# Kernel optimization log

Measured on AMD Instinct MI355X. Metric: run time of the kernel, lower is better.

## Reference

```python
import jax, jax.numpy as jnp
import numpy as np

H = 128          # hidden_channels
N_USER = 500000
N_ANIME = 20000
N_EDGE = 500000


def setup_inputs() -> dict:
    key = jax.random.key(0)
    k = jax.random.split(key, 8)
    s1 = 1.0 / np.sqrt(2 * H)   # torch Linear init scale (uniform bound)
    s2 = 1.0 / np.sqrt(H)
    return {
        "z_user": jax.random.normal(k[0], (N_USER, H), dtype=jnp.float32),
        "z_anime": jax.random.normal(k[1], (N_ANIME, H), dtype=jnp.float32),
        "row": jax.random.randint(k[2], (N_EDGE,), 0, N_USER, dtype=jnp.int64 if jax.config.jax_enable_x64 else jnp.int32),
        "col": jax.random.randint(k[3], (N_EDGE,), 0, N_ANIME, dtype=jnp.int64 if jax.config.jax_enable_x64 else jnp.int32),
        "W1": jax.random.uniform(k[4], (2 * H, H), minval=-s1, maxval=s1, dtype=jnp.float32),
        "b1": jnp.zeros((H,), dtype=jnp.float32),
        "W2": jax.random.uniform(k[5], (H, 1), minval=-s2, maxval=s2, dtype=jnp.float32),
        "b2": jnp.zeros((1,), dtype=jnp.float32),
    }


def reference(z_user, z_anime, row, col, W1, b1, W2, b2):
    zu = z_user[row]            # [E, H] gather
    za = z_anime[col]           # [E, H] gather
    # cat([zu, za], -1) @ W1 == zu @ W1[:H] + za @ W1[H:]  (avoids materializing concat)
    h = zu @ W1[:H] + za @ W1[H:] + b1          # [E, H]
    h = jax.nn.relu(h)
    out = h @ W2 + b2                            # [E, 1]
    return out.reshape(-1)
```

## Files before the change

### kernel.cpp

```cpp
#include <hip/hip_runtime.h>
#include <hip/hip_bf16.h>
#include <stdint.h>

#define H_ 128
#define THREADS 256
#define EDGES_PER_BLOCK 128

typedef __bf16 bf16x8 __attribute__((ext_vector_type(8)));
typedef float  f32x4  __attribute__((ext_vector_type(4)));


__device__ inline bf16x8 pack8(float4 a, float4 b) {
    bf16x8 v;
    v[0] = (__bf16)a.x; v[1] = (__bf16)a.y; v[2] = (__bf16)a.z; v[3] = (__bf16)a.w;
    v[4] = (__bf16)b.x; v[5] = (__bf16)b.y; v[6] = (__bf16)b.z; v[7] = (__bf16)b.w;
    return v;
}

__global__ void prep_kernel(const float* __restrict__ W1,
                            const float* __restrict__ za,
                            __bf16* __restrict__ wfrag,
                            __bf16* __restrict__ za_bf,
                            int nza) {
    int t = blockIdx.x * 256 + threadIdx.x;
    if (t < 32768) {
        int j  = t & 7;
        int ln = (t >> 3) & 63;
        int nt = (t >> 9) & 7;
        int ks = (t >> 12) & 7;
        int k  = ks * 32 + ((ln >> 4) << 3) + j;
        int n  = nt * 16 + (ln & 15);
        wfrag[t] = (__bf16)W1[k * H_ + n];
    } else {
        long i = (long)(t - 32768) * 8;
        if (i < nza) {
            float4 a = *(const float4*)(za + i);
            float4 b = *(const float4*)(za + i + 4);
            *(bf16x8*)(za_bf + i) = pack8(a, b);
        }
    }
}

__global__ __launch_bounds__(THREADS, 3)
void edge_decoder_kernel(const float* __restrict__ z_user,
                         const float* __restrict__ z_anime,
                         const int*   __restrict__ row,
                         const int*   __restrict__ col,
                         const float* __restrict__ W1,
                         const float* __restrict__ b1,
                         const float* __restrict__ W2,
                         const float* __restrict__ b2,
                         const __bf16* __restrict__ wfrag,
                         const __bf16* __restrict__ za_bf,
                         int use_ws,
                         float* __restrict__ out,
                         int E) {
    __shared__ bf16x8 Bf[4][8][64];

    const int tid  = threadIdx.x;
    const int lane = tid & 63;
    const int wv   = tid >> 6;
    const int g    = lane >> 4;
    const int m    = lane & 15;
    const int base = blockIdx.x * EDGES_PER_BLOCK + wv * 32;

    int e0 = base + m;        int e0c = e0 < E ? e0 : 0;
    int e1 = base + 16 + m;   int e1c = e1 < E ? e1 : 0;
    const int r0 = row[e0c], c0 = col[e0c];
    const int r1 = row[e1c], c1 = col[e1c];

    bf16x8 Au0[4], Au1[4];
    {
        const float* zu0 = z_user + (size_t)r0 * H_ + g * 8;
        const float* zu1 = z_user + (size_t)r1 * H_ + g * 8;
        #pragma unroll
        for (int ks = 0; ks < 4; ++ks) {
            float4 x0 = *(const float4*)(zu0 + ks * 32);
            float4 y0 = *(const float4*)(zu0 + ks * 32 + 4);
            float4 x1 = *(const float4*)(zu1 + ks * 32);
            float4 y1 = *(const float4*)(zu1 + ks * 32 + 4);
            Au0[ks] = pack8(x0, y0);
            Au1[ks] = pack8(x1, y1);
        }
    }

    if (use_ws) {
        const int4* src = (const int4*)wfrag;
        int4*       dst = (int4*)&Bf[0][0][0];
        #pragma unroll
        for (int i = 0; i < 8; ++i)
            dst[tid + i * THREADS] = src[tid + i * THREADS];
    } else {
        __bf16* d = (__bf16*)&Bf[0][0][0];
        for (int idx = tid; idx < H_ * H_; idx += THREADS) {
            int k = idx >> 7, n = idx & 127;
            int ks = k >> 5, gg = (k >> 3) & 3, j = k & 7;
            int nt = n >> 4, ln = (gg << 4) | (n & 15);
            d[ks * 4096 + nt * 512 + ln * 8 + j] = (__bf16)W1[k * H_ + n];
        }
    }
    __syncthreads();

    f32x4 acc0[8], acc1[8];
    #pragma unroll
    for (int nt = 0; nt < 8; ++nt) {
        acc0[nt] = (f32x4){0.f, 0.f, 0.f, 0.f};
        acc1[nt] = (f32x4){0.f, 0.f, 0.f, 0.f};
    }

    #pragma unroll
    for (int nt = 0; nt < 8; ++nt) {
        #pragma unroll
        for (int ks = 0; ks < 4; ++ks) {
            bf16x8 b = Bf[ks][nt][lane];
            acc0[nt] = __builtin_amdgcn_mfma_f32_16x16x32_bf16(Au0[ks], b, acc0[nt], 0, 0, 0);
            acc1[nt] = __builtin_amdgcn_mfma_f32_16x16x32_bf16(Au1[ks], b, acc1[nt], 0, 0, 0);
        }
    }

    bf16x8 Aa0[4], Aa1[4];
    if (use_ws) {
        const __bf16* za0 = za_bf + (size_t)c0 * H_ + g * 8;
        const __bf16* za1 = za_bf + (size_t)c1 * H_ + g * 8;
        #pragma unroll
        for (int ks = 0; ks < 4; ++ks) {
            Aa0[ks] = *(const bf16x8*)(za0 + ks * 32);
            Aa1[ks] = *(const bf16x8*)(za1 + ks * 32);
        }
    } else {
        const float* za0 = z_anime + (size_t)c0 * H_ + g * 8;
        const float* za1 = z_anime + (size_t)c1 * H_ + g * 8;
        #pragma unroll
        for (int ks = 0; ks < 4; ++ks) {
            float4 x0 = *(const float4*)(za0 + ks * 32);
            float4 y0 = *(const float4*)(za0 + ks * 32 + 4);
            float4 x1 = *(const float4*)(za1 + ks * 32);
            float4 y1 = *(const float4*)(za1 + ks * 32 + 4);
            Aa0[ks] = pack8(x0, y0);
            Aa1[ks] = pack8(x1, y1);
        }
    }

    __syncthreads();

    if (use_ws) {
        const int4* src = (const int4*)wfrag + 2048;
        int4*       dst = (int4*)&Bf[0][0][0];
        #pragma unroll
        for (int i = 0; i < 8; ++i)
            dst[tid + i * THREADS] = src[tid + i * THREADS];
    } else {
        __bf16* d = (__bf16*)&Bf[0][0][0];
        for (int idx = tid; idx < H_ * H_; idx += THREADS) {
            int k = idx >> 7, n = idx & 127;
            int ks = k >> 5, gg = (k >> 3) & 3, j = k & 7;
            int nt = n >> 4, ln = (gg << 4) | (n & 15);
            d[ks * 4096 + nt * 512 + ln * 8 + j] = (__bf16)W1[(H_ + k) * H_ + n];
        }
    }
    __syncthreads();

    #pragma unroll
    for (int nt = 0; nt < 8; ++nt) {
        #pragma unroll
        for (int ks = 0; ks < 4; ++ks) {
            bf16x8 b = Bf[ks][nt][lane];
            acc0[nt] = __builtin_amdgcn_mfma_f32_16x16x32_bf16(Aa0[ks], b, acc0[nt], 0, 0, 0);
            acc1[nt] = __builtin_amdgcn_mfma_f32_16x16x32_bf16(Aa1[ks], b, acc1[nt], 0, 0, 0);
        }
    }

    float w2v[8], b1v[8];
    #pragma unroll
    for (int nt = 0; nt < 8; ++nt) {
        int ch = nt * 16 + m;
        w2v[nt] = W2[ch];
        b1v[nt] = b1[ch];
    }
    const float bb = b2[0];

    #pragma unroll
    for (int tile = 0; tile < 2; ++tile) {
        float ps[4];
        #pragma unroll
        for (int r = 0; r < 4; ++r) {
            float s = 0.f;
            #pragma unroll
            for (int nt = 0; nt < 8; ++nt) {
                f32x4 a = tile ? acc1[nt] : acc0[nt];
                float h = a[r] + b1v[nt];
                s = fmaf(fmaxf(h, 0.f), w2v[nt], s);
            }
            ps[r] = s;
        }
        #pragma unroll
        for (int off = 1; off < 16; off <<= 1) {
            #pragma unroll
            for (int r = 0; r < 4; ++r)
                ps[r] += __shfl_xor(ps[r], off, 64);
        }
        if (m == 0) {
            int eb = base + tile * 16 + g * 4;
            if (eb < E) {
                float4 o = make_float4(ps[0] + bb, ps[1] + bb, ps[2] + bb, ps[3] + bb);
                *(float4*)(out + eb) = o;
            }
        }
    }
}

extern "C" void kernel_launch(void* const* d_in, const int* in_sizes, int n_in,
                              void* d_out, int out_size, void* d_ws, size_t ws_size,
                              hipStream_t stream) {
    const float* z_user  = (const float*)d_in[0];
    const float* z_anime = (const float*)d_in[1];
    const int*   row     = (const int*)d_in[2];
    const int*   col     = (const int*)d_in[3];
    const float* W1      = (const float*)d_in[4];
    const float* b1      = (const float*)d_in[5];
    const float* W2      = (const float*)d_in[6];
    const float* b2      = (const float*)d_in[7];
    float*       out     = (float*)d_out;
    const int E   = in_sizes[2];
    const int nza = in_sizes[1];

    const size_t wfrag_bytes = 2u * H_ * H_ * sizeof(__bf16);
    const size_t need = wfrag_bytes + (size_t)nza * sizeof(__bf16);
    int use_ws = (d_ws != nullptr && ws_size >= need) ? 1 : 0;

    __bf16* wfrag = (__bf16*)d_ws;
    __bf16* za_bf = (__bf16*)((char*)d_ws + wfrag_bytes);

    if (use_ws) {
        int za_threads = (nza + 7) / 8;
        int nb_prep = 128 + (za_threads + 255) / 256;
        prep_kernel<<<nb_prep, 256, 0, stream>>>(W1, z_anime, wfrag, za_bf, nza);
    }

    int nb = (E + EDGES_PER_BLOCK - 1) / EDGES_PER_BLOCK;
    edge_decoder_kernel<<<nb, THREADS, 0, stream>>>(
        z_user, z_anime, row, col, W1, b1, W2, b2, wfrag, za_bf, use_ws, out, E);
}
```

Before: 82.30 us.

## Bucket-sort edges by user row before decoding to improve gather locality

Adds a histogram, scan and scatter pass that reorders edges by coarse user-row bucket, then has the decoder read the permuted row/col indices and scatter outputs back through a permutation array. The aim is for each block's z_user gathers to land in nearby memory, improving cache and DRAM locality. In exchange it adds three extra launches, a memset, global atomics and scattered output writes. With uniformly random rows over a 256MB table, the locality gain may be small against the extra passes.

Measured after the change: 170.1 us. 2.07x slower.

```diff
diff --git a/kernel.cpp b/kernel.cpp
--- a/kernel.cpp
+++ b/kernel.cpp
@@ -5,6 +5,7 @@
 #define H_ 128
 #define THREADS 256
 #define EDGES_PER_BLOCK 128
+#define NBUCKET 4096
 
 typedef __bf16 bf16x8 __attribute__((ext_vector_type(8)));
 typedef float  f32x4  __attribute__((ext_vector_type(4)));
@@ -41,11 +42,67 @@
     }
 }
 
+__global__ void hist_kernel(const int* __restrict__ row, int* __restrict__ hist,
+                            int E, int shift) {
+    int i = blockIdx.x * blockDim.x + threadIdx.x;
+    int stride = gridDim.x * blockDim.x;
+    for (; i < E; i += stride)
+        atomicAdd(&hist[row[i] >> shift], 1);
+}
+
+__global__ __launch_bounds__(1024)
+void scan_kernel(int* __restrict__ h) {
+    __shared__ int wsum[16];
+    int tid = threadIdx.x;
+    int4 v = *(int4*)(h + tid * 4);
+    int s = v.x + v.y + v.z + v.w;
+    int lane = tid & 63, wv = tid >> 6;
+    int inc = s;
+    #pragma unroll
+    for (int off = 1; off < 64; off <<= 1) {
+        int t = __shfl_up(inc, off, 64);
+        if (lane >= off) inc += t;
+    }
+    if (lane == 63) wsum[wv] = inc;
+    __syncthreads();
+    if (wv == 0) {
+        int ws = (lane < 16) ? wsum[lane] : 0;
+        #pragma unroll
+        for (int off = 1; off < 16; off <<= 1) {
+            int t = __shfl_up(ws, off, 64);
+            if (lane >= off) ws += t;
+        }
+        if (lane < 16) wsum[lane] = ws;
+    }
+    __syncthreads();
+    int waveoff = (wv > 0) ? wsum[wv - 1] : 0;
+    int excl = waveoff + inc - s;
+    int4 o;
+    o.x = excl; o.y = excl + v.x; o.z = o.y + v.y; o.w = o.z + v.z;
+    *(int4*)(h + tid * 4) = o;
+}
+
+__global__ void scatter_kernel(const int* __restrict__ row, const int* __restrict__ col,
+                               int* __restrict__ hist,
+                               int* __restrict__ rowp, int* __restrict__ colp,
+                               int* __restrict__ perm, int E, int shift) {
+    int i = blockIdx.x * blockDim.x + threadIdx.x;
+    int stride = gridDim.x * blockDim.x;
+    for (; i < E; i += stride) {
+        int r = row[i], c = col[i];
+        int pos = atomicAdd(&hist[r >> shift], 1);
+        rowp[pos] = r;
+        colp[pos] = c;
+        perm[pos] = i;
+    }
+}
+
 __global__ __launch_bounds__(THREADS, 3)
 void edge_decoder_kernel(const float* __restrict__ z_user,
                          const float* __restrict__ z_anime,
-                         const int*   __restrict__ row,
-                         const int*   __restrict__ col,
+                         const int*   __restrict__ rowp,
+                         const int*   __restrict__ colp,
+                         const int*   __restrict__ perm,
                          const float* __restrict__ W1,
                          const float* __restrict__ b1,
                          const float* __restrict__ W2,
@@ -66,8 +123,8 @@
 
     int e0 = base + m;        int e0c = e0 < E ? e0 : 0;
     int e1 = base + 16 + m;   int e1c = e1 < E ? e1 : 0;
-    const int r0 = row[e0c], c0 = col[e0c];
-    const int r1 = row[e1c], c1 = col[e1c];
+    const int r0 = rowp[e0c], c0 = colp[e0c];
+    const int r1 = rowp[e1c], c1 = colp[e1c];
 
     bf16x8 Au0[4], Au1[4];
     {
@@ -201,7 +258,19 @@
         }
         if (m == 0) {
             int eb = base + tile * 16 + g * 4;
-            if (eb < E) {
+            if (perm) {
+                if (eb + 3 < E) {
+                    int4 p = *(const int4*)(perm + eb);
+                    out[p.x] = ps[0] + bb;
+                    out[p.y] = ps[1] + bb;
+                    out[p.z] = ps[2] + bb;
+                    out[p.w] = ps[3] + bb;
+                } else {
+                    #pragma unroll
+                    for (int r = 0; r < 4; ++r)
+                        if (eb + r < E) out[perm[eb + r]] = ps[r] + bb;
+                }
+            } else if (eb < E) {
                 float4 o = make_float4(ps[0] + bb, ps[1] + bb, ps[2] + bb, ps[3] + bb);
                 *(float4*)(out + eb) = o;
             }
@@ -223,21 +292,47 @@
     float*       out     = (float*)d_out;
     const int E   = in_sizes[2];
     const int nza = in_sizes[1];
+    const int nu  = in_sizes[0] / H_;
+
+    const int nb   = (E + EDGES_PER_BLOCK - 1) / EDGES_PER_BLOCK;
+    const int Epad = nb * EDGES_PER_BLOCK;
 
     const size_t wfrag_bytes = 2u * H_ * H_ * sizeof(__bf16);
-    const size_t need = wfrag_bytes + (size_t)nza * sizeof(__bf16);
+    const size_t za_bytes    = (size_t)nza * sizeof(__bf16);
+    const size_t hist_bytes  = (size_t)NBUCKET * sizeof(int);
+    const size_t idx_bytes   = (size_t)Epad * sizeof(int);
+    const size_t need = wfrag_bytes + za_bytes + hist_bytes + 3 * idx_bytes;
     int use_ws = (d_ws != nullptr && ws_size >= need) ? 1 : 0;
 
-    __bf16* wfrag = (__bf16*)d_ws;
-    __bf16* za_bf = (__bf16*)((char*)d_ws + wfrag_bytes);
+    char* p = (char*)d_ws;
+    __bf16* wfrag = (__bf16*)p;                 p += wfrag_bytes;
+    __bf16* za_bf = (__bf16*)p;                 p += za_bytes;
+    int*    hist  = (int*)p;                    p += hist_bytes;
+    int*    rowp  = (int*)p;                    p += idx_bytes;
+    int*    colp  = (int*)p;                    p += idx_bytes;
+    int*    perm  = (int*)p;
 
     if (use_ws) {
+        int shift = 0;
+        while ((nu >> shift) >= NBUCKET) shift++;
+
+        hipMemsetAsync(hist, 0, hist_bytes, stream);
+
         int za_threads = (nza + 7) / 8;
         int nb_prep = 128 + (za_threads + 255) / 256;
         prep_kernel<<<nb_prep, 256, 0, stream>>>(W1, z_anime, wfrag, za_bf, nza);
-    }
-
-    int nb = (E + EDGES_PER_BLOCK - 1) / EDGES_PER_BLOCK;
-    edge_decoder_kernel<<<nb, THREADS, 0, stream>>>(
-        z_user, z_anime, row, col, W1, b1, W2, b2, wfrag, za_bf, use_ws, out, E);
-}
+
+        int gsb = min(1024, (E + 255) / 256);
+        hist_kernel<<<gsb, 256, 0, stream>>>(row, hist, E, shift);
+        scan_kernel<<<1, 1024, 0, stream>>>(hist);
+        scatter_kernel<<<gsb, 256, 0, stream>>>(row, col, hist, rowp, colp, perm, E, shift);
+
+        edge_decoder_kernel<<<nb, THREADS, 0, stream>>>(
+            z_user, z_anime, rowp, colp, perm, W1, b1, W2, b2,
+            wfrag, za_bf, 1, out, E);
+    } else {
+        edge_decoder_kernel<<<nb, THREADS, 0, stream>>>(
+            z_user, z_anime, row, col, nullptr, W1, b1, W2, b2,
+            wfrag, za_bf, 0, out, E);
+    }
+}
```

## Persistent kernel with double-buffered async LDS gather of user embeddings

Applied to the files above, without the earlier changes.

Replaces the one-shot-per-block launch with a persistent grid of 256 blocks, 3 waves each. Every wave loops over 32-edge tiles and loads both W1 halves into LDS once. User rows are gathered asynchronously with global_load_lds into a swizzled, double-buffered LDS area, and row/col indices are prefetched two tiles ahead, so gather latency overlaps the MFMA work. The cost is fewer resident waves (launch bounds of 1, about 160KB of LDS), a full vmcnt(0) wait at the start of each iteration, and a fixed grid size that may not fill the device.

New measurement: 106.0 us. 1.29x slower.

```diff
diff --git a/kernel.cpp b/kernel.cpp
--- a/kernel.cpp
+++ b/kernel.cpp
@@ -3,8 +3,10 @@
 #include <stdint.h>
 
 #define H_ 128
-#define THREADS 256
-#define EDGES_PER_BLOCK 128
+#define NW 3
+#define THREADS (NW * 64)
+#define TILE_E 32
+#define NBLOCKS 256
 
 typedef __bf16 bf16x8 __attribute__((ext_vector_type(8)));
 typedef float  f32x4  __attribute__((ext_vector_type(4)));
@@ -41,7 +43,11 @@
     }
 }
 
-__global__ __launch_bounds__(THREADS, 3)
+#define GLD16(gp, lp) __builtin_amdgcn_global_load_lds(                      \
+    (const __attribute__((address_space(1))) void*)(gp),                     \
+    (__attribute__((address_space(3))) void*)(lp), 16, 0, 0)
+
+__global__ __launch_bounds__(THREADS, 1)
 void edge_decoder_kernel(const float* __restrict__ z_user,
                          const float* __restrict__ z_anime,
                          const int*   __restrict__ row,
@@ -55,44 +61,22 @@
                          int use_ws,
                          float* __restrict__ out,
                          int E) {
-    __shared__ bf16x8 Bf[4][8][64];
+    __shared__ bf16x8 Bf[8][8][64];
+    __shared__ float  ZU[NW][2][TILE_E * H_];
 
     const int tid  = threadIdx.x;
     const int lane = tid & 63;
     const int wv   = tid >> 6;
     const int g    = lane >> 4;
     const int m    = lane & 15;
-    const int base = blockIdx.x * EDGES_PER_BLOCK + wv * 32;
-
-    int e0 = base + m;        int e0c = e0 < E ? e0 : 0;
-    int e1 = base + 16 + m;   int e1c = e1 < E ? e1 : 0;
-    const int r0 = row[e0c], c0 = col[e0c];
-    const int r1 = row[e1c], c1 = col[e1c];
-
-    bf16x8 Au0[4], Au1[4];
-    {
-        const float* zu0 = z_user + (size_t)r0 * H_ + g * 8;
-        const float* zu1 = z_user + (size_t)r1 * H_ + g * 8;
-        #pragma unroll
-        for (int ks = 0; ks < 4; ++ks) {
-            float4 x0 = *(const float4*)(zu0 + ks * 32);
-            float4 y0 = *(const float4*)(zu0 + ks * 32 + 4);
-            float4 x1 = *(const float4*)(zu1 + ks * 32);
-            float4 y1 = *(const float4*)(zu1 + ks * 32 + 4);
-            Au0[ks] = pack8(x0, y0);
-            Au1[ks] = pack8(x1, y1);
-        }
-    }
 
     if (use_ws) {
         const int4* src = (const int4*)wfrag;
         int4*       dst = (int4*)&Bf[0][0][0];
-        #pragma unroll
-        for (int i = 0; i < 8; ++i)
-            dst[tid + i * THREADS] = src[tid + i * THREADS];
+        for (int i = tid; i < 4096; i += THREADS) dst[i] = src[i];
     } else {
         __bf16* d = (__bf16*)&Bf[0][0][0];
-        for (int idx = tid; idx < H_ * H_; idx += THREADS) {
+        for (int idx = tid; idx < 2 * H_ * H_; idx += THREADS) {
             int k = idx >> 7, n = idx & 127;
             int ks = k >> 5, gg = (k >> 3) & 3, j = k & 7;
             int nt = n >> 4, ln = (gg << 4) | (n & 15);
@@ -101,111 +85,175 @@
     }
     __syncthreads();
 
-    f32x4 acc0[8], acc1[8];
-    #pragma unroll
-    for (int nt = 0; nt < 8; ++nt) {
-        acc0[nt] = (f32x4){0.f, 0.f, 0.f, 0.f};
-        acc1[nt] = (f32x4){0.f, 0.f, 0.f, 0.f};
-    }
-
-    #pragma unroll
-    for (int nt = 0; nt < 8; ++nt) {
-        #pragma unroll
-        for (int ks = 0; ks < 4; ++ks) {
-            bf16x8 b = Bf[ks][nt][lane];
-            acc0[nt] = __builtin_amdgcn_mfma_f32_16x16x32_bf16(Au0[ks], b, acc0[nt], 0, 0, 0);
-            acc1[nt] = __builtin_amdgcn_mfma_f32_16x16x32_bf16(Au1[ks], b, acc1[nt], 0, 0, 0);
-        }
-    }
-
-    bf16x8 Aa0[4], Aa1[4];
-    if (use_ws) {
-        const __bf16* za0 = za_bf + (size_t)c0 * H_ + g * 8;
-        const __bf16* za1 = za_bf + (size_t)c1 * H_ + g * 8;
-        #pragma unroll
-        for (int ks = 0; ks < 4; ++ks) {
-            Aa0[ks] = *(const bf16x8*)(za0 + ks * 32);
-            Aa1[ks] = *(const bf16x8*)(za1 + ks * 32);
-        }
-    } else {
-        const float* za0 = z_anime + (size_t)c0 * H_ + g * 8;
-        const float* za1 = z_anime + (size_t)c1 * H_ + g * 8;
-        #pragma unroll
-        for (int ks = 0; ks < 4; ++ks) {
-            float4 x0 = *(const float4*)(za0 + ks * 32);
-            float4 y0 = *(const float4*)(za0 + ks * 32 + 4);
-            float4 x1 = *(const float4*)(za1 + ks * 32);
-            float4 y1 = *(const float4*)(za1 + ks * 32 + 4);
-            Aa0[ks] = pack8(x0, y0);
-            Aa1[ks] = pack8(x1, y1);
-        }
-    }
-
-    __syncthreads();
-
-    if (use_ws) {
-        const int4* src = (const int4*)wfrag + 2048;
-        int4*       dst = (int4*)&Bf[0][0][0];
-        #pragma unroll
-        for (int i = 0; i < 8; ++i)
-            dst[tid + i * THREADS] = src[tid + i * THREADS];
-    } else {
-        __bf16* d = (__bf16*)&Bf[0][0][0];
-        for (int idx = tid; idx < H_ * H_; idx += THREADS) {
-            int k = idx >> 7, n = idx & 127;
-            int ks = k >> 5, gg = (k >> 3) & 3, j = k & 7;
-            int nt = n >> 4, ln = (gg << 4) | (n & 15);
-            d[ks * 4096 + nt * 512 + ln * 8 + j] = (__bf16)W1[(H_ + k) * H_ + n];
-        }
-    }
-    __syncthreads();
-
-    #pragma unroll
-    for (int nt = 0; nt < 8; ++nt) {
-        #pragma unroll
-        for (int ks = 0; ks < 4; ++ks) {
-            bf16x8 b = Bf[ks][nt][lane];
-            acc0[nt] = __builtin_amdgcn_mfma_f32_16x16x32_bf16(Aa0[ks], b, acc0[nt], 0, 0, 0);
-            acc1[nt] = __builtin_amdgcn_mfma_f32_16x16x32_bf16(Aa1[ks], b, acc1[nt], 0, 0, 0);
-        }
-    }
-
     float w2v[8], b1v[8];
     #pragma unroll
-    for (int nt = 0; nt < 8; ++nt) {
-        int ch = nt * 16 + m;
-        w2v[nt] = W2[ch];
-        b1v[nt] = b1[ch];
-    }
+    for (int nt = 0; nt < 8; ++nt) { int ch = nt * 16 + m; w2v[nt] = W2[ch]; b1v[nt] = b1[ch]; }
     const float bb = b2[0];
 
-    #pragma unroll
-    for (int tile = 0; tile < 2; ++tile) {
-        float ps[4];
-        #pragma unroll
-        for (int r = 0; r < 4; ++r) {
-            float s = 0.f;
-            #pragma unroll
-            for (int nt = 0; nt < 8; ++nt) {
-                f32x4 a = tile ? acc1[nt] : acc0[nt];
-                float h = a[r] + b1v[nt];
-                s = fmaf(fmaxf(h, 0.f), w2v[nt], s);
-            }
-            ps[r] = s;
-        }
-        #pragma unroll
-        for (int off = 1; off < 16; off <<= 1) {
-            #pragma unroll
-            for (int r = 0; r < 4; ++r)
-                ps[r] += __shfl_xor(ps[r], off, 64);
-        }
-        if (m == 0) {
-            int eb = base + tile * 16 + g * 4;
-            if (eb < E) {
-                float4 o = make_float4(ps[0] + bb, ps[1] + bb, ps[2] + bb, ps[3] + bb);
-                *(float4*)(out + eb) = o;
-            }
-        }
+    const int T = (E + TILE_E - 1) / TILE_E;
+    const int NSTREAM = gridDim.x * NW;
+    int t = blockIdx.x * NW + wv;
+    if (t >= T) return;
+
+    float* zbuf0 = &ZU[wv][0][0];
+    float* zbuf1 = &ZU[wv][1][0];
+
+    int tb = t * TILE_E;
+    int ei = tb + (lane & 31); if (ei >= E) ei = E - 1;
+    int rv = row[ei];
+    int e0 = tb + m;      if (e0 >= E) e0 = E - 1;
+    int e1 = tb + 16 + m; if (e1 >= E) e1 = E - 1;
+    int ca0 = col[e0], ca1 = col[e1];
+
+    {
+        #pragma unroll
+        for (int i = 0; i < 16; ++i) {
+            int r0 = __builtin_amdgcn_readlane(rv, 2 * i);
+            int r1 = __builtin_amdgcn_readlane(rv, 2 * i + 1);
+            int r  = (lane < 32) ? r0 : r1;
+            int e  = 2 * i + (lane >> 5);
+            int c  = (lane & 31) ^ (e & 7);
+            GLD16(z_user + (size_t)r * H_ + c * 4, zbuf0 + i * 256);
+        }
+    }
+
+    int t1 = t + NSTREAM;
+    int tbn = (t1 < T ? t1 : 0) * TILE_E;
+    int en = tbn + (lane & 31); if (en >= E) en = E - 1;
+    int rv1 = row[en];
+    int f0 = tbn + m;      if (f0 >= E) f0 = E - 1;
+    int f1 = tbn + 16 + m; if (f1 >= E) f1 = E - 1;
+    int cb0 = col[f0], cb1 = col[f1];
+
+    int cur = 0;
+    while (true) {
+        asm volatile("s_waitcnt vmcnt(0)" ::: "memory");
+
+        const int nxt = t + NSTREAM;
+        const bool have_next = (nxt < T);
+        float* zb  = cur ? zbuf1 : zbuf0;
+        float* zbn = cur ? zbuf0 : zbuf1;
+
+        bf16x8 Aa0[4], Aa1[4];
+        if (use_ws) {
+            const __bf16* p0 = za_bf + (size_t)ca0 * H_ + g * 8;
+            const __bf16* p1 = za_bf + (size_t)ca1 * H_ + g * 8;
+            #pragma unroll
+            for (int ks = 0; ks < 4; ++ks) {
+                Aa0[ks] = *(const bf16x8*)(p0 + ks * 32);
+                Aa1[ks] = *(const bf16x8*)(p1 + ks * 32);
+            }
+        } else {
+            const float* p0 = z_anime + (size_t)ca0 * H_ + g * 8;
+            const float* p1 = z_anime + (size_t)ca1 * H_ + g * 8;
+            #pragma unroll
+            for (int ks = 0; ks < 4; ++ks) {
+                Aa0[ks] = pack8(*(const float4*)(p0 + ks * 32), *(const float4*)(p0 + ks * 32 + 4));
+                Aa1[ks] = pack8(*(const float4*)(p1 + ks * 32), *(const float4*)(p1 + ks * 32 + 4));
+            }
+        }
+
+        bf16x8 Au0[4], Au1[4];
+        {
+            const int swz = m & 7;
+            const float* r0p = zb + m * H_;
+            const float* r1p = zb + (m + 16) * H_;
+            #pragma unroll
+            for (int ks = 0; ks < 4; ++ks) {
+                int c0 = g * 2 + ks * 8;
+                float4 x0 = *(const float4*)(r0p + (((c0    ) ^ swz) << 2));
+                float4 y0 = *(const float4*)(r0p + (((c0 + 1) ^ swz) << 2));
+                float4 x1 = *(const float4*)(r1p + (((c0    ) ^ swz) << 2));
+                float4 y1 = *(const float4*)(r1p + (((c0 + 1) ^ swz) << 2));
+                Au0[ks] = pack8(x0, y0);
+                Au1[ks] = pack8(x1, y1);
+            }
+        }
+
+        if (have_next) {
+            #pragma unroll
+            for (int i = 0; i < 16; ++i) {
+                int r0 = __builtin_amdgcn_readlane(rv1, 2 * i);
+                int r1 = __builtin_amdgcn_readlane(rv1, 2 * i + 1);
+                int r  = (lane < 32) ? r0 : r1;
+                int e  = 2 * i + (lane >> 5);
+                int c  = (lane & 31) ^ (e & 7);
+                GLD16(z_user + (size_t)r * H_ + c * 4, zbn + i * 256);
+            }
+        }
+
+        int t2 = t + 2 * NSTREAM;
+        int tb2 = (t2 < T ? t2 : 0) * TILE_E;
+        int e2 = tb2 + (lane & 31); if (e2 >= E) e2 = E - 1;
+        int rv2 = row[e2];
+        int h0 = tb2 + m;      if (h0 >= E) h0 = E - 1;
+        int h1 = tb2 + 16 + m; if (h1 >= E) h1 = E - 1;
+        int cc0 = col[h0], cc1 = col[h1];
+
+        f32x4 acc0[8], acc1[8];
+        #pragma unroll
+        for (int nt = 0; nt < 8; ++nt) {
+            acc0[nt] = (f32x4){0.f, 0.f, 0.f, 0.f};
+            acc1[nt] = (f32x4){0.f, 0.f, 0.f, 0.f};
+        }
+        #pragma unroll
+        for (int nt = 0; nt < 8; ++nt) {
+            #pragma unroll
+            for (int ks = 0; ks < 4; ++ks) {
+                bf16x8 b = Bf[ks][nt][lane];
+                acc0[nt] = __builtin_amdgcn_mfma_f32_16x16x32_bf16(Au0[ks], b, acc0[nt], 0, 0, 0);
+                acc1[nt] = __builtin_amdgcn_mfma_f32_16x16x32_bf16(Au1[ks], b, acc1[nt], 0, 0, 0);
+            }
+        }
+        #pragma unroll
+        for (int nt = 0; nt < 8; ++nt) {
+            #pragma unroll
+            for (int ks = 0; ks < 4; ++ks) {
+                bf16x8 b = Bf[4 + ks][nt][lane];
+                acc0[nt] = __builtin_amdgcn_mfma_f32_16x16x32_bf16(Aa0[ks], b, acc0[nt], 0, 0, 0);
+                acc1[nt] = __builtin_amdgcn_mfma_f32_16x16x32_bf16(Aa1[ks], b, acc1[nt], 0, 0, 0);
+            }
+        }
+
+        int tb0 = t * TILE_E;
+        #pragma unroll
+        for (int tile = 0; tile < 2; ++tile) {
+            float ps[4];
+            #pragma unroll
+            for (int r = 0; r < 4; ++r) {
+                float s = 0.f;
+                #pragma unroll
+                for (int nt = 0; nt < 8; ++nt) {
+                    f32x4 a = tile ? acc1[nt] : acc0[nt];
+                    float h = a[r] + b1v[nt];
+                    s = fmaf(fmaxf(h, 0.f), w2v[nt], s);
+                }
+                ps[r] = s;
+            }
+            #pragma unroll
+            for (int off = 1; off < 16; off <<= 1) {
+                #pragma unroll
+                for (int r = 0; r < 4; ++r)
+                    ps[r] += __shfl_xor(ps[r], off, 64);
+            }
+            if (m == 0) {
+                int eb = tb0 + tile * 16 + g * 4;
+                if (eb + 3 < E) {
+                    float4 o = make_float4(ps[0] + bb, ps[1] + bb, ps[2] + bb, ps[3] + bb);
+                    *(float4*)(out + eb) = o;
+                } else {
+                    #pragma unroll
+                    for (int r = 0; r < 4; ++r)
+                        if (eb + r < E) out[eb + r] = ps[r] + bb;
+                }
+            }
+        }
+
+        if (!have_next) break;
+        t = nxt; cur ^= 1;
+        rv1 = rv2;
+        ca0 = cb0; ca1 = cb1;
+        cb0 = cc0; cb1 = cc1;
     }
 }
 
@@ -237,7 +285,7 @@
         prep_kernel<<<nb_prep, 256, 0, stream>>>(W1, z_anime, wfrag, za_bf, nza);
     }
 
-    int nb = (E + EDGES_PER_BLOCK - 1) / EDGES_PER_BLOCK;
-    edge_decoder_kernel<<<nb, THREADS, 0, stream>>>(
-        z_user, z_anime, row, col, W1, b1, W2, b2, wfrag, za_bf, use_ws, out, E);
-}
+    edge_decoder_kernel<<<NBLOCKS, THREADS, 0, stream>>>(
+        z_user, z_anime, row, col, W1, b1, W2, b2,
+        wfrag, za_bf, use_ws, out, E);
+}
```

## Halve edges per wave and issue all gathers before weight staging

Applied to the files above, without the earlier changes.

Each wave now handles one 16-edge tile instead of two, so each block covers 64 edges and the grid doubles. The z_user and bf16 z_anime gathers plus the bias and W2 loads are issued up front, before the shared-memory weight copy, to hide gather latency. The launch-bounds occupancy hint rises from 3 to 4. The cost is twice as many blocks, each restaging both 32 KB weight halves into LDS, which doubles weight traffic per edge. The tail store is fixed to write scalars when fewer than four edges remain.

Measured after the change: 78.23 us. 1.05x faster.

```diff
diff --git a/kernel.cpp b/kernel.cpp
--- a/kernel.cpp
+++ b/kernel.cpp
@@ -4,7 +4,7 @@
 
 #define H_ 128
 #define THREADS 256
-#define EDGES_PER_BLOCK 128
+#define EPB 64
 
 typedef __bf16 bf16x8 __attribute__((ext_vector_type(8)));
 typedef float  f32x4  __attribute__((ext_vector_type(4)));
@@ -41,7 +41,7 @@
     }
 }
 
-__global__ __launch_bounds__(THREADS, 3)
+__global__ __launch_bounds__(THREADS, 4)
 void edge_decoder_kernel(const float* __restrict__ z_user,
                          const float* __restrict__ z_anime,
                          const int*   __restrict__ row,
@@ -62,27 +62,32 @@
     const int wv   = tid >> 6;
     const int g    = lane >> 4;
     const int m    = lane & 15;
-    const int base = blockIdx.x * EDGES_PER_BLOCK + wv * 32;
-
-    int e0 = base + m;        int e0c = e0 < E ? e0 : 0;
-    int e1 = base + 16 + m;   int e1c = e1 < E ? e1 : 0;
-    const int r0 = row[e0c], c0 = col[e0c];
-    const int r1 = row[e1c], c1 = col[e1c];
-
-    bf16x8 Au0[4], Au1[4];
+    const int base = blockIdx.x * EPB + wv * 16;
+
+    int e = base + m; if (e >= E) e = E - 1;
+    const int r0 = row[e], c0 = col[e];
+
+    float4 xu[8];
     {
-        const float* zu0 = z_user + (size_t)r0 * H_ + g * 8;
-        const float* zu1 = z_user + (size_t)r1 * H_ + g * 8;
+        const float* zu = z_user + (size_t)r0 * H_ + g * 8;
         #pragma unroll
         for (int ks = 0; ks < 4; ++ks) {
-            float4 x0 = *(const float4*)(zu0 + ks * 32);
-            float4 y0 = *(const float4*)(zu0 + ks * 32 + 4);
-            float4 x1 = *(const float4*)(zu1 + ks * 32);
-            float4 y1 = *(const float4*)(zu1 + ks * 32 + 4);
-            Au0[ks] = pack8(x0, y0);
-            Au1[ks] = pack8(x1, y1);
-        }
-    }
+            xu[2 * ks]     = *(const float4*)(zu + ks * 32);
+            xu[2 * ks + 1] = *(const float4*)(zu + ks * 32 + 4);
+        }
+    }
+    bf16x8 Aa[4];
+    if (use_ws) {
+        const __bf16* za = za_bf + (size_t)c0 * H_ + g * 8;
+        #pragma unroll
+        for (int ks = 0; ks < 4; ++ks)
+            Aa[ks] = *(const bf16x8*)(za + ks * 32);
+    }
+
+    float w2v[8], b1v[8];
+    #pragma unroll
+    for (int nt = 0; nt < 8; ++nt) { int ch = nt * 16 + m; w2v[nt] = W2[ch]; b1v[nt] = b1[ch]; }
+    const float bb = b2[0];
 
     if (use_ws) {
         const int4* src = (const int4*)wfrag;
@@ -101,44 +106,30 @@
     }
     __syncthreads();
 
-    f32x4 acc0[8], acc1[8];
-    #pragma unroll
-    for (int nt = 0; nt < 8; ++nt) {
-        acc0[nt] = (f32x4){0.f, 0.f, 0.f, 0.f};
-        acc1[nt] = (f32x4){0.f, 0.f, 0.f, 0.f};
-    }
+    bf16x8 Au[4];
+    #pragma unroll
+    for (int ks = 0; ks < 4; ++ks)
+        Au[ks] = pack8(xu[2 * ks], xu[2 * ks + 1]);
+
+    f32x4 acc[8];
+    #pragma unroll
+    for (int nt = 0; nt < 8; ++nt) acc[nt] = (f32x4){0.f, 0.f, 0.f, 0.f};
 
     #pragma unroll
     for (int nt = 0; nt < 8; ++nt) {
         #pragma unroll
         for (int ks = 0; ks < 4; ++ks) {
             bf16x8 b = Bf[ks][nt][lane];
-            acc0[nt] = __builtin_amdgcn_mfma_f32_16x16x32_bf16(Au0[ks], b, acc0[nt], 0, 0, 0);
-            acc1[nt] = __builtin_amdgcn_mfma_f32_16x16x32_bf16(Au1[ks], b, acc1[nt], 0, 0, 0);
-        }
-    }
-
-    bf16x8 Aa0[4], Aa1[4];
-    if (use_ws) {
-        const __bf16* za0 = za_bf + (size_t)c0 * H_ + g * 8;
-        const __bf16* za1 = za_bf + (size_t)c1 * H_ + g * 8;
-        #pragma unroll
-        for (int ks = 0; ks < 4; ++ks) {
-            Aa0[ks] = *(const bf16x8*)(za0 + ks * 32);
-            Aa1[ks] = *(const bf16x8*)(za1 + ks * 32);
-        }
-    } else {
-        const float* za0 = z_anime + (size_t)c0 * H_ + g * 8;
-        const float* za1 = z_anime + (size_t)c1 * H_ + g * 8;
-        #pragma unroll
-        for (int ks = 0; ks < 4; ++ks) {
-            float4 x0 = *(const float4*)(za0 + ks * 32);
-            float4 y0 = *(const float4*)(za0 + ks * 32 + 4);
-            float4 x1 = *(const float4*)(za1 + ks * 32);
-            float4 y1 = *(const float4*)(za1 + ks * 32 + 4);
-            Aa0[ks] = pack8(x0, y0);
-            Aa1[ks] = pack8(x1, y1);
-        }
+            acc[nt] = __builtin_amdgcn_mfma_f32_16x16x32_bf16(Au[ks], b, acc[nt], 0, 0, 0);
+        }
+    }
+
+    if (!use_ws) {
+        const float* za = z_anime + (size_t)c0 * H_ + g * 8;
+        #pragma unroll
+        for (int ks = 0; ks < 4; ++ks)
+            Aa[ks] = pack8(*(const float4*)(za + ks * 32),
+                           *(const float4*)(za + ks * 32 + 4));
     }
 
     __syncthreads();
@@ -165,46 +156,36 @@
         #pragma unroll
         for (int ks = 0; ks < 4; ++ks) {
             bf16x8 b = Bf[ks][nt][lane];
-            acc0[nt] = __builtin_amdgcn_mfma_f32_16x16x32_bf16(Aa0[ks], b, acc0[nt], 0, 0, 0);
-            acc1[nt] = __builtin_amdgcn_mfma_f32_16x16x32_bf16(Aa1[ks], b, acc1[nt], 0, 0, 0);
-        }
-    }
-
-    float w2v[8], b1v[8];
-    #pragma unroll
-    for (int nt = 0; nt < 8; ++nt) {
-        int ch = nt * 16 + m;
-        w2v[nt] = W2[ch];
-        b1v[nt] = b1[ch];
-    }
-    const float bb = b2[0];
-
-    #pragma unroll
-    for (int tile = 0; tile < 2; ++tile) {
-        float ps[4];
-        #pragma unroll
-        for (int r = 0; r < 4; ++r) {
-            float s = 0.f;
-            #pragma unroll
-            for (int nt = 0; nt < 8; ++nt) {
-                f32x4 a = tile ? acc1[nt] : acc0[nt];
-                float h = a[r] + b1v[nt];
-                s = fmaf(fmaxf(h, 0.f), w2v[nt], s);
-            }
-            ps[r] = s;
-        }
-        #pragma unroll
-        for (int off = 1; off < 16; off <<= 1) {
+            acc[nt] = __builtin_amdgcn_mfma_f32_16x16x32_bf16(Aa[ks], b, acc[nt], 0, 0, 0);
+        }
+    }
+
+    float ps[4];
+    #pragma unroll
+    for (int r = 0; r < 4; ++r) {
+        float s = 0.f;
+        #pragma unroll
+        for (int nt = 0; nt < 8; ++nt) {
+            float h = acc[nt][r] + b1v[nt];
+            s = fmaf(fmaxf(h, 0.f), w2v[nt], s);
+        }
+        ps[r] = s;
+    }
+    #pragma unroll
+    for (int off = 1; off < 16; off <<= 1) {
+        #pragma unroll
+        for (int r = 0; r < 4; ++r)
+            ps[r] += __shfl_xor(ps[r], off, 64);
+    }
+    if (m == 0) {
+        int eb = base + g * 4;
+        if (eb + 3 < E) {
+            float4 o = make_float4(ps[0] + bb, ps[1] + bb, ps[2] + bb, ps[3] + bb);
+            *(float4*)(out + eb) = o;
+        } else {
             #pragma unroll
             for (int r = 0; r < 4; ++r)
-                ps[r] += __shfl_xor(ps[r], off, 64);
-        }
-        if (m == 0) {
-            int eb = base + tile * 16 + g * 4;
-            if (eb < E) {
-                float4 o = make_float4(ps[0] + bb, ps[1] + bb, ps[2] + bb, ps[3] + bb);
-                *(float4*)(out + eb) = o;
-            }
+                if (eb + r < E) out[eb + r] = ps[r] + bb;
         }
     }
 }
@@ -237,7 +218,8 @@
         prep_kernel<<<nb_prep, 256, 0, stream>>>(W1, z_anime, wfrag, za_bf, nza);
     }
 
-    int nb = (E + EDGES_PER_BLOCK - 1) / EDGES_PER_BLOCK;
+    int nb = (E + EPB - 1) / EPB;
     edge_decoder_kernel<<<nb, THREADS, 0, stream>>>(
-        z_user, z_anime, row, col, W1, b1, W2, b2, wfrag, za_bf, use_ws, out, E);
-}
+        z_user, z_anime, row, col, W1, b1, W2, b2,
+        wfrag, za_bf, use_ws, out, E);
+}
```
